# Optimization experiments

Measured on AMD Instinct MI355X. Metric: run time of the kernel, lower is better.

## Reference

```python
import jax, jax.numpy as jnp
from jax import lax
import numpy as np

B, H, W = 16, 512, 512
OPENING_R, EROSION_R, DILATION_R = 5, 2, 1
MIN_SIZE, AREA_THRESHOLD = 2000, 300
INF = np.int32(2 ** 30)


def _disk(r):
    # skimage.morphology.disk: x^2 + y^2 <= r^2 on a (2r+1)^2 grid
    y, x = np.mgrid[-r:r + 1, -r:r + 1]
    return jnp.asarray((x * x + y * y <= r * r).astype(np.float32))


D_OPEN, D_ERODE, D_DILATE = _disk(OPENING_R), _disk(EROSION_R), _disk(DILATION_R)


def _conv2(x, k):
    return lax.conv_general_dilated(x[None, None], k[None, None], (1, 1), 'VALID')[0, 0]


def _erode(fg, se):
    # skimage binary_erosion uses border_value=True (image border does not erode)
    r = se.shape[0] // 2
    x = jnp.pad(fg.astype(jnp.float32), r, constant_values=1.0)
    return _conv2(x, se) >= se.sum() - 0.5


def _dilate(fg, se):
    # skimage binary_dilation uses border_value=False
    r = se.shape[0] // 2
    x = jnp.pad(fg.astype(jnp.float32), r, constant_values=0.0)
    return _conv2(x, se) > 0.5


def _seg_cummin(v, reset, axis, reverse):
    # segmented cumulative-min: scan resets wherever `reset` is True (background)
    def comb(a, b):
        av, af = a
        bv, bf = b
        return jnp.where(bf, bv, jnp.minimum(av, bv)), af | bf

    vv, _ = lax.associative_scan(comb, (v, reset), axis=axis, reverse=reverse)
    return vv


def _label(fg):
    # 4-connectivity connected-component labeling via min-label propagation.
    # Each fg pixel starts with its raveled index; alternating row/col segmented
    # cummin sweeps run under while_loop until a fixed point (root id per comp).
    h, w = fg.shape
    idx = jnp.arange(h * w, dtype=jnp.int32).reshape(h, w)
    lab0 = jnp.where(fg, idx, INF)
    bg = ~fg

    def sweep(l):
        for axis in (1, 0):
            for rev in (False, True):
                l = jnp.where(fg, _seg_cummin(l, bg, axis, rev), INF)
        return l

    def body(c):
        l, _ = c
        nl = sweep(l)
        return nl, jnp.array_equal(nl, l)

    lab, _ = lax.while_loop(lambda c: ~c[1], body, (lab0, jnp.array(False)))
    seg = jnp.where(fg, lab, 0).ravel()
    sizes = jax.ops.segment_sum(fg.astype(jnp.int32).ravel(), seg, num_segments=h * w)
    ncomp = jnp.sum(sizes > 0)
    return lab, sizes, ncomp


def _remove_small_objects(fg, min_size, guard):
    lab, sizes, ncomp = _label(fg)
    px = sizes[jnp.where(fg, lab, 0)]  # component size at every fg pixel
    kept = fg & (px >= min_size)
    # original only removes small objects when label(...).max() > 1
    return jnp.where(ncomp > 1, kept, fg) if guard else kept


def _pipeline(mask):
    fg = mask > 0
    fg = _remove_small_objects(fg, MIN_SIZE, True)
    # remove_small_holes == ~remove_small_objects(~fg, area_threshold + 1)
    fg = ~_remove_small_objects(~fg, AREA_THRESHOLD + 1, False)
    fg = _erode(fg, D_ERODE)
    fg = _dilate(_erode(fg, D_OPEN), D_OPEN)  # binary_opening
    fg = _remove_small_objects(fg, MIN_SIZE, True)
    fg = _dilate(fg, D_DILATE)
    return fg.astype(jnp.float32)  # original casts to int; float32 kept for vjp parity


def setup_inputs() -> dict:
    key = jax.random.key(0)
    # blobby binary masks: threshold bilinearly-upsampled low-res noise so that
    # realistic large connected components (> min_size px) exist
    low = jax.random.uniform(key, (B, H // 16, W // 16), dtype=jnp.float32)
    blob = jax.image.resize(low, (B, H, W), method='bilinear')
    return {'inputs': (blob > 0.5).astype(jnp.float32)}


def reference(inputs):
    return jax.vmap(_pipeline)(inputs)
```

## Files before the change

### kernel.cpp

```cpp
#include <hip/hip_runtime.h>
#include <stdint.h>

#define BATCH 16
#define H 512
#define W 512
#define HW (H * W)
#define NTOT (BATCH * HW)
#define NWORDS (NTOT / 64)

#define SROWS 16
#define SWORDS 128
#define SPIX 8192
#define NSTRIPS (NWORDS / SWORDS)
#define IMG_STRIPS 32

#define MAXR 4096
#define NR (NSTRIPS * MAXR)

#define SPIN_LIMIT (1 << 20)

__device__ int g_flags[BATCH * 32];

__device__ __forceinline__ int ald(const int* p) {
    return __hip_atomic_load((int*)p, __ATOMIC_RELAXED, __HIP_MEMORY_SCOPE_AGENT);
}
__device__ __forceinline__ void ast(int* p, int v) {
    __hip_atomic_store(p, v, __ATOMIC_RELAXED, __HIP_MEMORY_SCOPE_AGENT);
}
__device__ __forceinline__ uint64_t ald64(const uint64_t* p) {
    return __hip_atomic_load((uint64_t*)p, __ATOMIC_RELAXED, __HIP_MEMORY_SCOPE_AGENT);
}
__device__ __forceinline__ void ast64(uint64_t* p, uint64_t v) {
    __hip_atomic_store(p, v, __ATOMIC_RELAXED, __HIP_MEMORY_SCOPE_AGENT);
}

__device__ __forceinline__ int find_root_c(int* L, int x) {
    int r = x, p = ald(&L[r]);
    while (p != r) { r = p; p = ald(&L[r]); }
    if (ald(&L[x]) != r) atomicMin(&L[x], r);
    return r;
}

__device__ void merge_uf(int* L, int a, int b) {
    while (true) {
        a = find_root_c(L, a);
        b = find_root_c(L, b);
        if (a == b) return;
        int lo = a < b ? a : b;
        int hi = a < b ? b : a;
        int old = atomicMin(&L[hi], lo);
        if (old == hi) return;
        a = lo; b = old;
    }
}

__device__ __forceinline__ int find_root_lds(int* P, int x) {
    int r = x, p = P[r];
    while (p != r) { r = p; p = P[r]; }
    return r;
}

__device__ void merge_lds(int* P, int a, int b) {
    while (true) {
        a = find_root_lds(P, a);
        b = find_root_lds(P, b);
        if (a == b) return;
        int lo = a < b ? a : b;
        int hi = a < b ? b : a;
        int old = atomicMin(&P[hi], lo);
        if (old == hi) return;
        a = lo; b = old;
    }
}

__device__ __forceinline__ int run_of(uint64_t m, int i, int cvrid, int wr) {
    uint64_t below = i ? ((~m) & ((1ull << i) - 1)) : 0ull;
    if (below == 0) return (cvrid >= 0) ? cvrid : wr;
    int s = 64 - __builtin_clzll(below);
    uint64_t starts = m & ~((m << 1) | ((cvrid >= 0) ? 1ull : 0ull));
    return wr + __popcll(starts & ((1ull << s) - 1));
}

__device__ __forceinline__ int run_of_lds(uint64_t m, int i, int cvrid,
                                          uint64_t starts, int wb) {
    uint64_t below = i ? ((~m) & ((1ull << i) - 1)) : 0ull;
    if (below == 0) return (cvrid >= 0) ? cvrid : wb;
    int s = 64 - __builtin_clzll(below);
    return wb + __popcll(starts & ((1ull << s) - 1));
}

__device__ __forceinline__ void hash_add(int* hk, int* hv, int* sizes,
                                         int r, int cnt) {
    uint32_t h = ((uint32_t)r * 2654435761u) >> 25;
    for (int tt = 0; tt < 16; ++tt) {
        int slot = (h + tt) & 127;
        int k = hk[slot];
        if (k == -1) k = atomicCAS(&hk[slot], -1, r);
        if (k == -1 || k == r) { atomicAdd(&hv[slot], cnt); return; }
    }
    atomicAdd(&sizes[r], cnt);
}

__device__ uint64_t keep_core(uint64_t m, int cvg, int wrg, int nc,
                              const int* L, const int* sizes, int minsz) {
    uint64_t res = m;
    if (!m) return res;
    uint64_t rem = m;
    uint64_t pc[4]; int rd[4];
    int rk = 0;
#pragma unroll
    for (int k = 0; k < 4; ++k) {
        pc[k] = 0; rd[k] = wrg;
        if (rem) {
            int s = __builtin_ctzll(rem);
            uint64_t rest = rem >> s;
            uint64_t nr = ~rest;
            int len = nr ? __builtin_ctzll(nr) : (64 - s);
            uint64_t piece = ((len >= 64) ? ~0ull : ((1ull << len) - 1)) << s;
            bool initial = !(s == 0 && cvg >= 0);
            pc[k] = piece;
            rd[k] = initial ? (wrg + rk) : cvg;
            rk += initial ? 1 : 0;
            rem &= ~piece;
        }
    }
    int rt[4], sz[4];
#pragma unroll
    for (int k = 0; k < 4; ++k) rt[k] = ald(&L[rd[k]]);
#pragma unroll
    for (int k = 0; k < 4; ++k) {
        int idx = pc[k] ? rt[k] : rd[k];
        sz[k] = ald(&sizes[idx]);
    }
    if (nc > 1) {
#pragma unroll
        for (int k = 0; k < 4; ++k)
            if (pc[k] && sz[k] < minsz) res &= ~pc[k];
        while (rem) {
            int s = __builtin_ctzll(rem);
            uint64_t rest = rem >> s;
            uint64_t nr = ~rest;
            int len = nr ? __builtin_ctzll(nr) : (64 - s);
            uint64_t piece = ((len >= 64) ? ~0ull : ((1ull << len) - 1)) << s;
            int rid = wrg + rk++;
            if (ald(&sizes[ald(&L[rid])]) < minsz) res &= ~piece;
            rem &= ~piece;
        }
    }
    return res;
}

__device__ uint64_t fill_core(uint64_t fg, int cvg, int wrg,
                              const int* L, const int* sizes, int minsz) {
    uint64_t bg = ~fg;
    uint64_t res = fg;
    if (!bg) return res;
    uint64_t rem = bg;
    uint64_t pc[4]; int rd[4];
    int rk = 0;
#pragma unroll
    for (int k = 0; k < 4; ++k) {
        pc[k] = 0; rd[k] = wrg;
        if (rem) {
            int s = __builtin_ctzll(rem);
            uint64_t rest = rem >> s;
            uint64_t nr = ~rest;
            int len = nr ? __builtin_ctzll(nr) : (64 - s);
            uint64_t piece = ((len >= 64) ? ~0ull : ((1ull << len) - 1)) << s;
            bool initial = !(s == 0 && cvg >= 0);
            pc[k] = piece;
            rd[k] = initial ? (wrg + rk) : cvg;
            rk += initial ? 1 : 0;
            rem &= ~piece;
        }
    }
    int rt[4], sz[4];
#pragma unroll
    for (int k = 0; k < 4; ++k) rt[k] = ald(&L[rd[k]]);
#pragma unroll
    for (int k = 0; k < 4; ++k) {
        int idx = pc[k] ? rt[k] : rd[k];
        sz[k] = ald(&sizes[idx]);
    }
#pragma unroll
    for (int k = 0; k < 4; ++k)
        if (pc[k] && sz[k] < minsz) res |= pc[k];
    while (rem) {
        int s = __builtin_ctzll(rem);
        uint64_t rest = rem >> s;
        uint64_t nr = ~rest;
        int len = nr ? __builtin_ctzll(nr) : (64 - s);
        uint64_t piece = ((len >= 64) ? ~0ull : ((1ull << len) - 1)) << s;
        int rid = wrg + rk++;
        if (ald(&sizes[ald(&L[rid])]) < minsz) res |= piece;
        rem &= ~piece;
    }
    return res;
}

__device__ void flatten_fast(uint64_t m, int cvg, int wrg,
                             int* L, int* sizes, int* ncomp_img,
                             int t, int* hk, int* hv) {
    if (t < 128) { hk[t] = -1; hv[t] = 0; }
    __syncthreads();
    if (t < SWORDS && m) {
        uint64_t rem = m;
        uint64_t pc[4]; int rd[4]; bool ini[4];
        int rk = 0;
#pragma unroll
        for (int k = 0; k < 4; ++k) {
            pc[k] = 0; rd[k] = wrg; ini[k] = false;
            if (rem) {
                int s = __builtin_ctzll(rem);
                uint64_t rest = rem >> s;
                uint64_t nr = ~rest;
                int len = nr ? __builtin_ctzll(nr) : (64 - s);
                uint64_t piece = ((len >= 64) ? ~0ull : ((1ull << len) - 1)) << s;
                bool initial = !(s == 0 && cvg >= 0);
                pc[k] = piece;
                rd[k] = initial ? (wrg + rk) : cvg;
                ini[k] = initial;
                rk += initial ? 1 : 0;
                rem &= ~piece;
            }
        }
        int h1[4], h2[4];
#pragma unroll
        for (int k = 0; k < 4; ++k) h1[k] = ald(&L[rd[k]]);
#pragma unroll
        for (int k = 0; k < 4; ++k) {
            int i1 = pc[k] ? h1[k] : rd[k];
            h2[k] = ald(&L[i1]);
        }
#pragma unroll
        for (int k = 0; k < 4; ++k) {
            if (pc[k]) {
                int r;
                if (h2[k] == h1[k]) r = h1[k];
                else {
                    r = h2[k];
                    int p = ald(&L[r]);
                    while (p != r) { r = p; p = ald(&L[r]); }
                }
                if (h1[k] != r) atomicMin(&L[rd[k]], r);
                if (ini[k] && r == rd[k]) atomicAdd(ncomp_img, 1);
                hash_add(hk, hv, sizes, r, __popcll(pc[k]));
            }
        }
        while (rem) {
            int s = __builtin_ctzll(rem);
            uint64_t rest = rem >> s;
            uint64_t nr = ~rest;
            int len = nr ? __builtin_ctzll(nr) : (64 - s);
            uint64_t piece = ((len >= 64) ? ~0ull : ((1ull << len) - 1)) << s;
            int rid = wrg + rk++;
            int r = find_root_c(L, rid);
            if (r == rid) atomicAdd(ncomp_img, 1);
            hash_add(hk, hv, sizes, r, __popcll(piece));
            rem &= ~piece;
        }
    }
    __syncthreads();
    if (t < 128 && hk[t] != -1) atomicAdd(&sizes[hk[t]], hv[t]);
}

template <int R, bool ERODE>
__device__ uint64_t morph_word_lds(const uint64_t* buf, int lrow, int w, int gyTop) {
    const uint64_t BORDER = ERODE ? ~0ull : 0ull;
    uint64_t res = ERODE ? ~0ull : 0ull;
#pragma unroll
    for (int dy = -R; dy <= R; ++dy) {
        int lr = lrow + dy;
        int gy = gyTop + lr;
        if (gy < 0 || gy >= H) continue;
        int v = R * R - dy * dy;
        int kx = 0;
        while ((kx + 1) * (kx + 1) <= v) ++kx;
        uint64_t cur = buf[lr * 8 + w];
        uint64_t prv = (w > 0) ? buf[lr * 8 + w - 1] : BORDER;
        uint64_t nxt = (w < 7) ? buf[lr * 8 + w + 1] : BORDER;
        uint64_t acc = cur;
#pragma unroll
        for (int dx = 1; dx <= kx; ++dx) {
            uint64_t right = (cur >> dx) | (nxt << (64 - dx));
            uint64_t left  = (cur << dx) | (prv >> (64 - dx));
            if (ERODE) acc &= right & left;
            else       acc |= right | left;
        }
        if (ERODE) res &= acc;
        else       res |= acc;
    }
    return res;
}

__device__ void strip_ccl_body(uint64_t m, uint64_t* sw, int* scarry,
                               int* cntL, int* wbL, int* par,
                               int blk, int t,
                               int* __restrict__ carry, int* __restrict__ wordrun,
                               int* __restrict__ L, int* __restrict__ sizes,
                               int* __restrict__ ncomp) {
    if (t < SWORDS) sw[t] = m;
    __syncthreads();

    if (t < SWORDS) {
        bool cont = (t & 7) ? ((sw[t - 1] >> 63) != 0) : false;
        int c = __popcll(m & ~(m << 1));
        if ((m & 1ull) && cont) --c;
        cntL[t] = c;
        wbL[t] = c;
    }
    __syncthreads();
    for (int off = 1; off < SWORDS; off <<= 1) {
        int v = 0;
        if (t < SWORDS && t >= off) v = wbL[t - off];
        __syncthreads();
        if (t < SWORDS) wbL[t] += v;
        __syncthreads();
    }

    if (t < SROWS) {
        int cv = -1;
        for (int i = 0; i < 8; ++i) {
            int lw = t * 8 + i;
            scarry[lw] = cv;
            uint64_t w = sw[lw];
            if (w >> 63) { if (cntL[lw] > 0) cv = wbL[lw] - 1; }
            else cv = -1;
        }
    }
    for (int i = t; i < MAXR; i += 256) par[i] = i;
    __syncthreads();

    int cv = -1, wb = 0;
    uint64_t starts = 0ull;
    if (t < SWORDS) {
        cv = scarry[t];
        wb = wbL[t] - cntL[t];
        ast(&carry[blk * SWORDS + t], (cv >= 0) ? (blk * MAXR + cv) : -1);
        ast(&wordrun[blk * SWORDS + t], blk * MAXR + wb);
        starts = m & ~((m << 1) | ((cv >= 0) ? 1ull : 0ull));
    }
    __syncthreads();

    if (t >= 8 && t < SWORDS && m) {
        uint64_t up = sw[t - 8];
        uint64_t cand = m & up;
        if (cand) {
            uint64_t curprev = (t & 7) ? sw[t - 1] : 0ull;
            uint64_t upprev  = (t & 7) ? sw[t - 9] : 0ull;
            uint64_t curl = (m << 1) | (curprev >> 63);
            uint64_t upl  = (up << 1) | (upprev >> 63);
            cand &= ~(curl & upl);
            int cvu = scarry[t - 8];
            int wbu = wbL[t - 8] - cntL[t - 8];
            uint64_t startsU = up & ~((up << 1) | ((cvu >= 0) ? 1ull : 0ull));
            while (cand) {
                int i = __builtin_ctzll(cand);
                int sP = run_of_lds(m, i, cv, starts, wb);
                int sQ = run_of_lds(up, i, cvu, startsU, wbu);
                merge_lds(par, sP, sQ);
                cand &= cand - 1;
            }
        }
    }
    __syncthreads();

    if (t < SWORDS) {
        int g = blk * MAXR;
        uint64_t ss = starts;
        int rk = 0;
        while (ss) {
            int rid = wb + rk; ++rk;
            int r = find_root_lds(par, rid);
            ast(&L[g + rid], g + r);
            if (r == rid) ast(&sizes[g + rid], 0);
            ss &= ss - 1;
        }
    }
    if (t == 0 && (blk & 31) == 0) ast(&ncomp[blk >> 5], 0);
}

__device__ __forceinline__ void ibar(int img, int si, int ep, int phase) {
    int* base = g_flags + img * 32;
    __syncthreads();
    if (threadIdx.x == 0) {
        asm volatile("s_waitcnt vmcnt(0)" ::: "memory");
        ast(&base[si], ep + phase);
    }
    if (threadIdx.x < 32) {
        int spins = 0;
        while (ald(&base[threadIdx.x]) - ep < phase && ++spins < SPIN_LIMIT)
            __builtin_amdgcn_s_sleep(1);
    }
    __syncthreads();
}

__global__ __launch_bounds__(256, 2) void k_mega(
        const float4* __restrict__ in4, float* __restrict__ out,
        int* LA, int* sizesA, int* LB, int* sizesB,
        uint64_t* bits1, uint64_t* bits2, uint64_t* bits3,
        int* carryA, int* carryB, int* wordrunA, int* wordrunB,
        int* ncompA, int* ncompB) {
    __shared__ uint64_t sw[SWORDS];
    __shared__ int scarry[SWORDS];
    __shared__ int cntL[SWORDS];
    __shared__ int wbL[SWORDS];
    __shared__ union US {
        int par[MAXR];
        struct { uint64_t A[320]; uint64_t B[320]; } mo;
        struct { int hk[128]; int hv[128]; } ha;
        struct { uint64_t kb[80]; uint64_t db[64]; } kd;
    } U;
    int blk = blockIdx.x;
    int t = threadIdx.x;
    int img = blk >> 5, si = blk & 31;
    int ep = ald(&g_flags[img * 32 + si]);

#pragma unroll
    for (int it = 0; it < 8; ++it) {
        int q = blk * (SPIX / 4) + it * 256 + t;
        float4 v = in4[q];
        uint32_t nib = (v.x > 0.0f ? 1u : 0u) | (v.y > 0.0f ? 2u : 0u) |
                       (v.z > 0.0f ? 4u : 0u) | (v.w > 0.0f ? 8u : 0u);
        uint64_t val = (uint64_t)nib << (4 * (t & 15));
        val |= __shfl_xor(val, 1);
        val |= __shfl_xor(val, 2);
        val |= __shfl_xor(val, 4);
        val |= __shfl_xor(val, 8);
        if ((t & 15) == 0) {
            ast64(&bits1[q >> 4], val);
            sw[it * 16 + (t >> 4)] = val;
        }
    }
    __syncthreads();

    {
        uint64_t m = (t < SWORDS) ? sw[t] : 0ull;
        strip_ccl_body(m, sw, scarry, cntL, wbL, U.par, blk, t,
                       carryA, wordrunA, LA, sizesA, ncompA);
    }
    ibar(img, si, ep, 1);

    if (t < 8 && si < 31) {
        int gw = (blk + 1) * SWORDS + t;
        uint64_t cur = ald64(&bits1[gw]);
        uint64_t curprev = t ? ald64(&bits1[gw - 1]) : 0ull;
        int cvc = ald(&carryA[gw]);
        int wrc = ald(&wordrunA[gw]);
        uint64_t up = sw[120 + t];
        uint64_t upprev = t ? sw[119 + t] : 0ull;
        int cvuL = scarry[120 + t];
        int cvu = cvuL >= 0 ? blk * MAXR + cvuL : -1;
        int wru = blk * MAXR + (wbL[120 + t] - cntL[120 + t]);
        uint64_t cand = cur & up;
        if (cand) {
            uint64_t curl = (cur << 1) | (curprev >> 63);
            uint64_t upl  = (up << 1) | (upprev >> 63);
            cand &= ~(curl & upl);
            while (cand) {
                int i = __builtin_ctzll(cand);
                int sP = run_of(cur, i, cvc, wrc);
                int sQ = run_of(up, i, cvu, wru);
                merge_uf(LA, sP, sQ);
                cand &= cand - 1;
            }
        }
    }
    ibar(img, si, ep, 2);

    {
        uint64_t m = (t < SWORDS) ? sw[t] : 0ull;
        int cvL = (t < SWORDS) ? scarry[t] : -1;
        int cvg = cvL >= 0 ? blk * MAXR + cvL : -1;
        int wrg = blk * MAXR + ((t < SWORDS) ? (wbL[t] - cntL[t]) : 0);
        flatten_fast(m, cvg, wrg, LA, sizesA, &ncompA[img], t, U.ha.hk, U.ha.hv);
    }
    ibar(img, si, ep, 3);

    {
        uint64_t m2 = 0ull;
        if (t < SWORDS) {
            int nc = ald(&ncompA[img]);
            uint64_t m1 = sw[t];
            int cvL = scarry[t];
            int cvg = cvL >= 0 ? blk * MAXR + cvL : -1;
            int wrg = blk * MAXR + (wbL[t] - cntL[t]);
            uint64_t kw = keep_core(m1, cvg, wrg, nc, LA, sizesA, 2000);
            ast64(&bits2[blk * SWORDS + t], kw);
            m2 = ~kw;
        }
        strip_ccl_body(m2, sw, scarry, cntL, wbL, U.par, blk, t,
                       carryB, wordrunB, LB, sizesB, ncompB);
    }
    ibar(img, si, ep, 4);

    if (t < 8 && si < 31) {
        int gw = (blk + 1) * SWORDS + t;
        uint64_t cur = ~ald64(&bits2[gw]);
        uint64_t curprev = t ? ~ald64(&bits2[gw - 1]) : 0ull;
        int cvc = ald(&carryB[gw]);
        int wrc = ald(&wordrunB[gw]);
        uint64_t up = sw[120 + t];
        uint64_t upprev = t ? sw[119 + t] : 0ull;
        int cvuL = scarry[120 + t];
        int cvu = cvuL >= 0 ? blk * MAXR + cvuL : -1;
        int wru = blk * MAXR + (wbL[120 + t] - cntL[120 + t]);
        uint64_t cand = cur & up;
        if (cand) {
            uint64_t curl = (cur << 1) | (curprev >> 63);
            uint64_t upl  = (up << 1) | (upprev >> 63);
            cand &= ~(curl & upl);
            while (cand) {
                int i = __builtin_ctzll(cand);
                int sP = run_of(cur, i, cvc, wrc);
                int sQ = run_of(up, i, cvu, wru);
                merge_uf(LB, sP, sQ);
                cand &= cand - 1;
            }
        }
    }
    ibar(img, si, ep, 5);

    {
        uint64_t m = (t < SWORDS) ? sw[t] : 0ull;
        int cvL = (t < SWORDS) ? scarry[t] : -1;
        int cvg = cvL >= 0 ? blk * MAXR + cvL : -1;
        int wrg = blk * MAXR + ((t < SWORDS) ? (wbL[t] - cntL[t]) : 0);
        flatten_fast(m, cvg, wrg, LB, sizesB, &ncompB[img], t, U.ha.hk, U.ha.hv);
    }
    ibar(img, si, ep, 6);

    {
        int gyTop = si * 16 - 12;
        for (int lw = t; lw < 320; lw += 256) {
            int gy = gyTop + (lw >> 3);
            int w = lw & 7;
            uint64_t v = 0;
            if (gy >= 0 && gy < H) {
                uint64_t fg; int cvg, wrg;
                if (lw >= 96 && lw < 224) {
                    int ti = lw - 96;
                    fg = ~sw[ti];
                    int cvL = scarry[ti];
                    cvg = cvL >= 0 ? blk * MAXR + cvL : -1;
                    wrg = blk * MAXR + (wbL[ti] - cntL[ti]);
                } else {
                    int gw = img * 4096 + gy * 8 + w;
                    fg = ald64(&bits2[gw]);
                    cvg = ald(&carryB[gw]);
                    wrg = ald(&wordrunB[gw]);
                }
                v = fill_core(fg, cvg, wrg, LB, sizesB, 301);
            }
            U.mo.A[lw] = v;
        }
        __syncthreads();
        for (int lw = t; lw < 320; lw += 256) {
            int lr = lw >> 3;
            if (lr >= 2 && lr <= 37) U.mo.B[lw] = morph_word_lds<2, true>(U.mo.A, lr, lw & 7, gyTop);
        }
        __syncthreads();
        for (int lw = t; lw < 320; lw += 256) {
            int lr = lw >> 3;
            if (lr >= 7 && lr <= 32) U.mo.A[lw] = morph_word_lds<5, true>(U.mo.B, lr, lw & 7, gyTop);
        }
        __syncthreads();
        for (int lw = t; lw < 320; lw += 256) {
            int lr = lw >> 3;
            if (lr >= 12 && lr <= 27) U.mo.B[lw] = morph_word_lds<5, false>(U.mo.A, lr, lw & 7, gyTop);
        }
        __syncthreads();
        uint64_t m3 = 0ull;
        if (t < SWORDS) {
            m3 = U.mo.B[t + 96];
            ast64(&bits3[blk * SWORDS + t], m3);
        }
        strip_ccl_body(m3, sw, scarry, cntL, wbL, U.par, blk, t,
                       carryA, wordrunA, LA, sizesA, ncompA);
    }
    ibar(img, si, ep, 7);

    if (t < 8 && si < 31) {
        int gw = (blk + 1) * SWORDS + t;
        uint64_t cur = ald64(&bits3[gw]);
        uint64_t curprev = t ? ald64(&bits3[gw - 1]) : 0ull;
        int cvc = ald(&carryA[gw]);
        int wrc = ald(&wordrunA[gw]);
        uint64_t up = sw[120 + t];
        uint64_t upprev = t ? sw[119 + t] : 0ull;
        int cvuL = scarry[120 + t];
        int cvu = cvuL >= 0 ? blk * MAXR + cvuL : -1;
        int wru = blk * MAXR + (wbL[120 + t] - cntL[120 + t]);
        uint64_t cand = cur & up;
        if (cand) {
            uint64_t curl = (cur << 1) | (curprev >> 63);
            uint64_t upl  = (up << 1) | (upprev >> 63);
            cand &= ~(curl & upl);
            while (cand) {
                int i = __builtin_ctzll(cand);
                int sP = run_of(cur, i, cvc, wrc);
                int sQ = run_of(up, i, cvu, wru);
                merge_uf(LA, sP, sQ);
                cand &= cand - 1;
            }
        }
    }
    ibar(img, si, ep, 8);

    {
        uint64_t m = (t < SWORDS) ? sw[t] : 0ull;
        int cvL = (t < SWORDS) ? scarry[t] : -1;
        int cvg = cvL >= 0 ? blk * MAXR + cvL : -1;
        int wrg = blk * MAXR + ((t < SWORDS) ? (wbL[t] - cntL[t]) : 0);
        flatten_fast(m, cvg, wrg, LA, sizesA, &ncompA[img], t, U.ha.hk, U.ha.hv);
    }
    ibar(img, si, ep, 9);

    for (int k = 0; k < 2; ++k) {
        int s8 = 2 * si + k;
        int y0 = s8 * 8;
        if (t < 80) {
            int lr = t >> 3, w = t & 7;
            int gy = y0 - 1 + lr;
            uint64_t v = 0;
            if (gy >= 0 && gy < H) {
                int nc = ald(&ncompA[img]);
                uint64_t m; int cvg, wrg;
                int rel = gy - 16 * si;
                if (rel >= 0 && rel < 16) {
                    int ti = rel * 8 + w;
                    m = sw[ti];
                    int cvL = scarry[ti];
                    cvg = cvL >= 0 ? blk * MAXR + cvL : -1;
                    wrg = blk * MAXR + (wbL[ti] - cntL[ti]);
                } else {
                    int gw = img * 4096 + gy * 8 + w;
                    m = ald64(&bits3[gw]);
                    cvg = ald(&carryA[gw]);
                    wrg = ald(&wordrunA[gw]);
                }
                v = keep_core(m, cvg, wrg, nc, LA, sizesA, 2000);
            }
            U.kd.kb[t] = v;
        }
        __syncthreads();
        if (t < 64) {
            int r = t >> 3, w = t & 7;
            uint64_t cur = U.kd.kb[(r + 1) * 8 + w];
            uint64_t up  = U.kd.kb[r * 8 + w];
            uint64_t dn  = U.kd.kb[(r + 2) * 8 + w];
            uint64_t prv = w ? U.kd.kb[(r + 1) * 8 + w - 1] : 0ull;
            uint64_t nxt = (w < 7) ? U.kd.kb[(r + 1) * 8 + w + 1] : 0ull;
            U.kd.db[t] = cur | up | dn | (cur << 1) | (prv >> 63) |
                         (cur >> 1) | (nxt << 63);
        }
        __syncthreads();
        {
            int q0 = t * 16;
            uint64_t wd = U.kd.db[q0 >> 6];
            int sh = q0 & 63;
            float4* o = (float4*)(out + (size_t)img * HW + (size_t)y0 * W + q0);
#pragma unroll
            for (int kk = 0; kk < 4; ++kk) {
                uint32_t nib = (uint32_t)(wd >> (sh + kk * 4)) & 0xFu;
                float4 f;
                f.x = (nib & 1u) ? 1.0f : 0.0f;
                f.y = (nib & 2u) ? 1.0f : 0.0f;
                f.z = (nib & 4u) ? 1.0f : 0.0f;
                f.w = (nib & 8u) ? 1.0f : 0.0f;
                o[kk] = f;
            }
        }
        __syncthreads();
    }
}

extern "C" void kernel_launch(void* const* d_in, const int* in_sizes, int n_in,
                              void* d_out, int out_size, void* d_ws, size_t ws_size,
                              hipStream_t stream) {
    const float* in = (const float*)d_in[0];
    float* out = (float*)d_out;

    uint8_t* ws = (uint8_t*)d_ws;
    int* LA      = (int*)ws;
    int* sizesA  = LA + NR;
    int* LB      = sizesA + NR;
    int* sizesB  = LB + NR;
    uint64_t* bits1 = (uint64_t*)(sizesB + NR);
    uint64_t* bits2 = bits1 + NWORDS;
    uint64_t* bits3 = bits2 + NWORDS;
    int* carryA   = (int*)(bits3 + NWORDS);
    int* carryB   = carryA + NWORDS;
    int* wordrunA = carryB + NWORDS;
    int* wordrunB = wordrunA + NWORDS;
    int* ncompA   = wordrunB + NWORDS;
    int* ncompB   = ncompA + BATCH;

    k_mega<<<NSTRIPS, 256, 0, stream>>>((const float4*)in, out,
                                        LA, sizesA, LB, sizesB,
                                        bits1, bits2, bits3,
                                        carryA, carryB, wordrunA, wordrunB,
                                        ncompA, ncompB);
}
```

Before: 189.8 us.

## Keep local union-find parents in LDS and cache per-root sizes in shared hash

The strip-local parent array now has its own shared-memory buffer and survives past the local CCL step. Flattening, keep and fill passes resolve each run's local root in LDS and look up its global root and size through a 256-slot shared hash. The hash is filled once per strip, replacing per-run global loads of labels and sizes. Halo rows keep the global path. Bounded walk limits were added to the find loops. The cost is extra LDS footprint that may lower occupancy, plus more barriers.

```diff
diff --git a/kernel.cpp b/kernel.cpp
--- a/kernel.cpp
+++ b/kernel.cpp
@@ -18,6 +18,7 @@
 #define NR (NSTRIPS * MAXR)
 
 #define SPIN_LIMIT (1 << 20)
+#define WALK_LIMIT (1 << 16)
 
 __device__ int g_flags[BATCH * 32];
 
@@ -35,14 +36,21 @@
 }
 
 __device__ __forceinline__ int find_root_c(int* L, int x) {
-    int r = x, p = ald(&L[r]);
-    while (p != r) { r = p; p = ald(&L[r]); }
+    int r = x, p = ald(&L[r]), g = 0;
+    while (p != r && ++g < WALK_LIMIT) { r = p; p = ald(&L[r]); }
     if (ald(&L[x]) != r) atomicMin(&L[x], r);
     return r;
 }
 
+__device__ __forceinline__ int walk_root(const int* L, int x) {
+    int r = x, p = ald(&L[r]), g = 0;
+    while (p != r && ++g < WALK_LIMIT) { r = p; p = ald(&L[r]); }
+    return r;
+}
+
 __device__ void merge_uf(int* L, int a, int b) {
-    while (true) {
+    int g = 0;
+    while (++g < WALK_LIMIT) {
         a = find_root_c(L, a);
         b = find_root_c(L, b);
         if (a == b) return;
@@ -54,14 +62,15 @@
     }
 }
 
-__device__ __forceinline__ int find_root_lds(int* P, int x) {
-    int r = x, p = P[r];
-    while (p != r) { r = p; p = P[r]; }
+__device__ __forceinline__ int find_root_lds(const int* P, int x) {
+    int r = x, p = P[r], g = 0;
+    while (p != r && ++g < WALK_LIMIT) { r = p; p = P[r]; }
     return r;
 }
 
 __device__ void merge_lds(int* P, int a, int b) {
-    while (true) {
+    int g = 0;
+    while (++g < WALK_LIMIT) {
         a = find_root_lds(P, a);
         b = find_root_lds(P, b);
         if (a == b) return;
@@ -89,179 +98,163 @@
     return wb + __popcll(starts & ((1ull << s) - 1));
 }
 
-__device__ __forceinline__ void hash_add(int* hk, int* hv, int* sizes,
-                                         int r, int cnt) {
-    uint32_t h = ((uint32_t)r * 2654435761u) >> 25;
-    for (int tt = 0; tt < 16; ++tt) {
-        int slot = (h + tt) & 127;
-        int k = hk[slot];
-        if (k == -1) k = atomicCAS(&hk[slot], -1, r);
-        if (k == -1 || k == r) { atomicAdd(&hv[slot], cnt); return; }
-    }
-    atomicAdd(&sizes[r], cnt);
-}
-
-__device__ uint64_t keep_core(uint64_t m, int cvg, int wrg, int nc,
-                              const int* L, const int* sizes, int minsz) {
-    uint64_t res = m;
-    if (!m) return res;
-    uint64_t rem = m;
-    uint64_t pc[4]; int rd[4];
-    int rk = 0;
-#pragma unroll
-    for (int k = 0; k < 4; ++k) {
-        pc[k] = 0; rd[k] = wrg;
-        if (rem) {
-            int s = __builtin_ctzll(rem);
-            uint64_t rest = rem >> s;
-            uint64_t nr = ~rest;
-            int len = nr ? __builtin_ctzll(nr) : (64 - s);
-            uint64_t piece = ((len >= 64) ? ~0ull : ((1ull << len) - 1)) << s;
-            bool initial = !(s == 0 && cvg >= 0);
-            pc[k] = piece;
-            rd[k] = initial ? (wrg + rk) : cvg;
-            rk += initial ? 1 : 0;
-            rem &= ~piece;
-        }
-    }
-    int rt[4], sz[4];
-#pragma unroll
-    for (int k = 0; k < 4; ++k) rt[k] = ald(&L[rd[k]]);
-#pragma unroll
-    for (int k = 0; k < 4; ++k) {
-        int idx = pc[k] ? rt[k] : rd[k];
-        sz[k] = ald(&sizes[idx]);
-    }
-    if (nc > 1) {
-#pragma unroll
-        for (int k = 0; k < 4; ++k)
-            if (pc[k] && sz[k] < minsz) res &= ~pc[k];
+__device__ __forceinline__ int hash_insert(int key, int cnt, int* hk, int* hcnt) {
+    uint32_t h = ((uint32_t)key * 2654435761u) >> 24;
+    for (int p = 0; p < 16; ++p) {
+        int s = (h + p) & 255;
+        int k = hk[s];
+        if (k == -1) k = atomicCAS(&hk[s], -1, key);
+        if (k == -1 || k == key) { atomicAdd(&hcnt[s], cnt); return s; }
+    }
+    return -1;
+}
+__device__ __forceinline__ int hash_find(int key, const int* hk) {
+    uint32_t h = ((uint32_t)key * 2654435761u) >> 24;
+    for (int p = 0; p < 16; ++p) {
+        int s = (h + p) & 255;
+        if (hk[s] == key) return s;
+        if (hk[s] == -1) return -1;
+    }
+    return -1;
+}
+
+__device__ void flatten_map(uint64_t m, int cvL, int wb, const int* par,
+                            int gbase, int* L, int* sizes, int* ncomp_img,
+                            int t, int* hk, int* hcnt, int* hrs) {
+    for (int i = t; i < 256; i += 256) { hk[i] = -1; hcnt[i] = 0; }
+    __syncthreads();
+    if (t < SWORDS && m) {
+        uint64_t rem = m; int rk = 0;
         while (rem) {
             int s = __builtin_ctzll(rem);
             uint64_t rest = rem >> s;
             uint64_t nr = ~rest;
             int len = nr ? __builtin_ctzll(nr) : (64 - s);
             uint64_t piece = ((len >= 64) ? ~0ull : ((1ull << len) - 1)) << s;
-            int rid = wrg + rk++;
-            if (ald(&sizes[ald(&L[rid])]) < minsz) res &= ~piece;
+            bool ini = !(s == 0 && cvL >= 0);
+            int rl = ini ? (wb + rk) : cvL; rk += ini ? 1 : 0;
+            int rloc = find_root_lds(par, rl);
+            int cnt = __popcll(piece);
+            if (hash_insert(rloc, cnt, hk, hcnt) < 0)
+                atomicAdd(&sizes[find_root_c(L, gbase + rloc)], cnt);
             rem &= ~piece;
         }
     }
-    return res;
-}
-
-__device__ uint64_t fill_core(uint64_t fg, int cvg, int wrg,
-                              const int* L, const int* sizes, int minsz) {
-    uint64_t bg = ~fg;
-    uint64_t res = fg;
-    if (!bg) return res;
-    uint64_t rem = bg;
-    uint64_t pc[4]; int rd[4];
-    int rk = 0;
-#pragma unroll
-    for (int k = 0; k < 4; ++k) {
-        pc[k] = 0; rd[k] = wrg;
-        if (rem) {
+    __syncthreads();
+    if (t < 256 && hk[t] != -1) {
+        int g = gbase + hk[t];
+        int r = find_root_c(L, g);
+        hrs[t] = r;
+        atomicAdd(&sizes[r], hcnt[t]);
+    }
+    __syncthreads();
+    if (t < SWORDS && m) {
+        uint64_t rem = m; int rk = 0;
+        while (rem) {
             int s = __builtin_ctzll(rem);
             uint64_t rest = rem >> s;
             uint64_t nr = ~rest;
             int len = nr ? __builtin_ctzll(nr) : (64 - s);
             uint64_t piece = ((len >= 64) ? ~0ull : ((1ull << len) - 1)) << s;
-            bool initial = !(s == 0 && cvg >= 0);
-            pc[k] = piece;
-            rd[k] = initial ? (wrg + rk) : cvg;
-            rk += initial ? 1 : 0;
+            bool ini = !(s == 0 && cvL >= 0);
+            if (ini) {
+                int rl = wb + rk;
+                int rloc = find_root_lds(par, rl);
+                int sl = hash_find(rloc, hk);
+                int r = (sl >= 0) ? hrs[sl] : walk_root(L, gbase + rloc);
+                ast(&L[gbase + rl], r);
+                if (r == gbase + rl) atomicAdd(ncomp_img, 1);
+                ++rk;
+            }
             rem &= ~piece;
         }
     }
-    int rt[4], sz[4];
-#pragma unroll
-    for (int k = 0; k < 4; ++k) rt[k] = ald(&L[rd[k]]);
-#pragma unroll
-    for (int k = 0; k < 4; ++k) {
-        int idx = pc[k] ? rt[k] : rd[k];
-        sz[k] = ald(&sizes[idx]);
-    }
-#pragma unroll
-    for (int k = 0; k < 4; ++k)
-        if (pc[k] && sz[k] < minsz) res |= pc[k];
+}
+
+__device__ __forceinline__ void preload_sv(const int* sizes, int t,
+                                           const int* hk, const int* hrs, int* hsv) {
+    if (t < 256 && hk[t] != -1) hsv[t] = ald(&sizes[hrs[t]]);
+}
+
+__device__ uint64_t keep_map(uint64_t m, int cvL, int wb, const int* par, int gbase,
+                             const int* L, const int* sizes, int minsz,
+                             const int* hk, const int* hrs, const int* hsv) {
+    uint64_t res = m, rem = m; int rk = 0;
     while (rem) {
         int s = __builtin_ctzll(rem);
         uint64_t rest = rem >> s;
         uint64_t nr = ~rest;
         int len = nr ? __builtin_ctzll(nr) : (64 - s);
         uint64_t piece = ((len >= 64) ? ~0ull : ((1ull << len) - 1)) << s;
-        int rid = wrg + rk++;
-        if (ald(&sizes[ald(&L[rid])]) < minsz) res |= piece;
+        bool ini = !(s == 0 && cvL >= 0);
+        int rl = ini ? (wb + rk) : cvL; rk += ini ? 1 : 0;
+        int rloc = find_root_lds(par, rl);
+        int sl = hash_find(rloc, hk);
+        int sz = (sl >= 0) ? hsv[sl] : ald(&sizes[walk_root(L, gbase + rloc)]);
+        if (sz < minsz) res &= ~piece;
         rem &= ~piece;
     }
     return res;
 }
 
-__device__ void flatten_fast(uint64_t m, int cvg, int wrg,
-                             int* L, int* sizes, int* ncomp_img,
-                             int t, int* hk, int* hv) {
-    if (t < 128) { hk[t] = -1; hv[t] = 0; }
-    __syncthreads();
-    if (t < SWORDS && m) {
-        uint64_t rem = m;
-        uint64_t pc[4]; int rd[4]; bool ini[4];
-        int rk = 0;
-#pragma unroll
-        for (int k = 0; k < 4; ++k) {
-            pc[k] = 0; rd[k] = wrg; ini[k] = false;
-            if (rem) {
-                int s = __builtin_ctzll(rem);
-                uint64_t rest = rem >> s;
-                uint64_t nr = ~rest;
-                int len = nr ? __builtin_ctzll(nr) : (64 - s);
-                uint64_t piece = ((len >= 64) ? ~0ull : ((1ull << len) - 1)) << s;
-                bool initial = !(s == 0 && cvg >= 0);
-                pc[k] = piece;
-                rd[k] = initial ? (wrg + rk) : cvg;
-                ini[k] = initial;
-                rk += initial ? 1 : 0;
-                rem &= ~piece;
-            }
-        }
-        int h1[4], h2[4];
-#pragma unroll
-        for (int k = 0; k < 4; ++k) h1[k] = ald(&L[rd[k]]);
-#pragma unroll
-        for (int k = 0; k < 4; ++k) {
-            int i1 = pc[k] ? h1[k] : rd[k];
-            h2[k] = ald(&L[i1]);
-        }
-#pragma unroll
-        for (int k = 0; k < 4; ++k) {
-            if (pc[k]) {
-                int r;
-                if (h2[k] == h1[k]) r = h1[k];
-                else {
-                    r = h2[k];
-                    int p = ald(&L[r]);
-                    while (p != r) { r = p; p = ald(&L[r]); }
-                }
-                if (h1[k] != r) atomicMin(&L[rd[k]], r);
-                if (ini[k] && r == rd[k]) atomicAdd(ncomp_img, 1);
-                hash_add(hk, hv, sizes, r, __popcll(pc[k]));
-            }
-        }
+__device__ uint64_t fill_map(uint64_t fg, int cvL, int wb, const int* par, int gbase,
+                             const int* L, const int* sizes, int minsz,
+                             const int* hk, const int* hrs, const int* hsv) {
+    uint64_t bg = ~fg;
+    uint64_t res = fg, rem = bg; int rk = 0;
+    while (rem) {
+        int s = __builtin_ctzll(rem);
+        uint64_t rest = rem >> s;
+        uint64_t nr = ~rest;
+        int len = nr ? __builtin_ctzll(nr) : (64 - s);
+        uint64_t piece = ((len >= 64) ? ~0ull : ((1ull << len) - 1)) << s;
+        bool ini = !(s == 0 && cvL >= 0);
+        int rl = ini ? (wb + rk) : cvL; rk += ini ? 1 : 0;
+        int rloc = find_root_lds(par, rl);
+        int sl = hash_find(rloc, hk);
+        int sz = (sl >= 0) ? hsv[sl] : ald(&sizes[walk_root(L, gbase + rloc)]);
+        if (sz < minsz) res |= piece;
+        rem &= ~piece;
+    }
+    return res;
+}
+
+__device__ uint64_t keep_halo(uint64_t m, int cvg, int wrg, int nc,
+                              const int* L, const int* sizes, int minsz) {
+    uint64_t res = m;
+    if (m && nc > 1) {
+        uint64_t rem = m; int rk = 0;
         while (rem) {
             int s = __builtin_ctzll(rem);
             uint64_t rest = rem >> s;
             uint64_t nr = ~rest;
             int len = nr ? __builtin_ctzll(nr) : (64 - s);
             uint64_t piece = ((len >= 64) ? ~0ull : ((1ull << len) - 1)) << s;
-            int rid = wrg + rk++;
-            int r = find_root_c(L, rid);
-            if (r == rid) atomicAdd(ncomp_img, 1);
-            hash_add(hk, hv, sizes, r, __popcll(piece));
+            bool ini = !(s == 0 && cvg >= 0);
+            int rid = ini ? (wrg + rk) : cvg; rk += ini ? 1 : 0;
+            if (ald(&sizes[ald(&L[rid])]) < minsz) res &= ~piece;
             rem &= ~piece;
         }
     }
-    __syncthreads();
-    if (t < 128 && hk[t] != -1) atomicAdd(&sizes[hk[t]], hv[t]);
+    return res;
+}
+__device__ uint64_t fill_halo(uint64_t fg, int cvg, int wrg,
+                              const int* L, const int* sizes, int minsz) {
+    uint64_t bg = ~fg;
+    uint64_t res = fg;
+    uint64_t rem = bg; int rk = 0;
+    while (rem) {
+        int s = __builtin_ctzll(rem);
+        uint64_t rest = rem >> s;
+        uint64_t nr = ~rest;
+        int len = nr ? __builtin_ctzll(nr) : (64 - s);
+        uint64_t piece = ((len >= 64) ? ~0ull : ((1ull << len) - 1)) << s;
+        bool ini = !(s == 0 && cvg >= 0);
+        int rid = ini ? (wrg + rk) : cvg; rk += ini ? 1 : 0;
+        if (ald(&sizes[ald(&L[rid])]) < minsz) res |= piece;
+        rem &= ~piece;
+    }
+    return res;
 }
 
 template <int R, bool ERODE>
@@ -405,15 +398,17 @@
     __shared__ int scarry[SWORDS];
     __shared__ int cntL[SWORDS];
     __shared__ int wbL[SWORDS];
+    __shared__ int hk[256], hcnt[256], hrs[256], hsv[256];
+    __shared__ int shnc;
+    __shared__ int parS[MAXR];
     __shared__ union US {
-        int par[MAXR];
         struct { uint64_t A[320]; uint64_t B[320]; } mo;
-        struct { int hk[128]; int hv[128]; } ha;
         struct { uint64_t kb[80]; uint64_t db[64]; } kd;
     } U;
     int blk = blockIdx.x;
     int t = threadIdx.x;
     int img = blk >> 5, si = blk & 31;
+    int gb = blk * MAXR;
     int ep = ald(&g_flags[img * 32 + si]);
 
 #pragma unroll
@@ -436,7 +431,7 @@
 
     {
         uint64_t m = (t < SWORDS) ? sw[t] : 0ull;
-        strip_ccl_body(m, sw, scarry, cntL, wbL, U.par, blk, t,
+        strip_ccl_body(m, sw, scarry, cntL, wbL, parS, blk, t,
                        carryA, wordrunA, LA, sizesA, ncompA);
     }
     ibar(img, si, ep, 1);
@@ -450,8 +445,8 @@
         uint64_t up = sw[120 + t];
         uint64_t upprev = t ? sw[119 + t] : 0ull;
         int cvuL = scarry[120 + t];
-        int cvu = cvuL >= 0 ? blk * MAXR + cvuL : -1;
-        int wru = blk * MAXR + (wbL[120 + t] - cntL[120 + t]);
+        int cvu = cvuL >= 0 ? gb + cvuL : -1;
+        int wru = gb + (wbL[120 + t] - cntL[120 + t]);
         uint64_t cand = cur & up;
         if (cand) {
             uint64_t curl = (cur << 1) | (curprev >> 63);
@@ -471,25 +466,29 @@
     {
         uint64_t m = (t < SWORDS) ? sw[t] : 0ull;
         int cvL = (t < SWORDS) ? scarry[t] : -1;
-        int cvg = cvL >= 0 ? blk * MAXR + cvL : -1;
-        int wrg = blk * MAXR + ((t < SWORDS) ? (wbL[t] - cntL[t]) : 0);
-        flatten_fast(m, cvg, wrg, LA, sizesA, &ncompA[img], t, U.ha.hk, U.ha.hv);
+        int wb = (t < SWORDS) ? (wbL[t] - cntL[t]) : 0;
+        flatten_map(m, cvL, wb, parS, gb, LA, sizesA, &ncompA[img],
+                    t, hk, hcnt, hrs);
     }
     ibar(img, si, ep, 3);
 
     {
+        if (t == 0) shnc = ald(&ncompA[img]);
+        preload_sv(sizesA, t, hk, hrs, hsv);
+        __syncthreads();
         uint64_t m2 = 0ull;
         if (t < SWORDS) {
-            int nc = ald(&ncompA[img]);
             uint64_t m1 = sw[t];
             int cvL = scarry[t];
-            int cvg = cvL >= 0 ? blk * MAXR + cvL : -1;
-            int wrg = blk * MAXR + (wbL[t] - cntL[t]);
-            uint64_t kw = keep_core(m1, cvg, wrg, nc, LA, sizesA, 2000);
+            int wb = wbL[t] - cntL[t];
+            uint64_t kw = (shnc > 1)
+                ? keep_map(m1, cvL, wb, parS, gb, LA, sizesA, 2000, hk, hrs, hsv)
+                : m1;
             ast64(&bits2[blk * SWORDS + t], kw);
             m2 = ~kw;
         }
-        strip_ccl_body(m2, sw, scarry, cntL, wbL, U.par, blk, t,
+        __syncthreads();
+        strip_ccl_body(m2, sw, scarry, cntL, wbL, parS, blk, t,
                        carryB, wordrunB, LB, sizesB, ncompB);
     }
     ibar(img, si, ep, 4);
@@ -503,8 +502,8 @@
         uint64_t up = sw[120 + t];
         uint64_t upprev = t ? sw[119 + t] : 0ull;
         int cvuL = scarry[120 + t];
-        int cvu = cvuL >= 0 ? blk * MAXR + cvuL : -1;
-        int wru = blk * MAXR + (wbL[120 + t] - cntL[120 + t]);
+        int cvu = cvuL >= 0 ? gb + cvuL : -1;
+        int wru = gb + (wbL[120 + t] - cntL[120 + t]);
         uint64_t cand = cur & up;
         if (cand) {
             uint64_t curl = (cur << 1) | (curprev >> 63);
@@ -524,33 +523,35 @@
     {
         uint64_t m = (t < SWORDS) ? sw[t] : 0ull;
         int cvL = (t < SWORDS) ? scarry[t] : -1;
-        int cvg = cvL >= 0 ? blk * MAXR + cvL : -1;
-        int wrg = blk * MAXR + ((t < SWORDS) ? (wbL[t] - cntL[t]) : 0);
-        flatten_fast(m, cvg, wrg, LB, sizesB, &ncompB[img], t, U.ha.hk, U.ha.hv);
+        int wb = (t < SWORDS) ? (wbL[t] - cntL[t]) : 0;
+        flatten_map(m, cvL, wb, parS, gb, LB, sizesB, &ncompB[img],
+                    t, hk, hcnt, hrs);
     }
     ibar(img, si, ep, 6);
 
     {
+        preload_sv(sizesB, t, hk, hrs, hsv);
+        __syncthreads();
         int gyTop = si * 16 - 12;
         for (int lw = t; lw < 320; lw += 256) {
             int gy = gyTop + (lw >> 3);
             int w = lw & 7;
             uint64_t v = 0;
             if (gy >= 0 && gy < H) {
-                uint64_t fg; int cvg, wrg;
                 if (lw >= 96 && lw < 224) {
                     int ti = lw - 96;
-                    fg = ~sw[ti];
+                    uint64_t fg = ~sw[ti];
                     int cvL = scarry[ti];
-                    cvg = cvL >= 0 ? blk * MAXR + cvL : -1;
-                    wrg = blk * MAXR + (wbL[ti] - cntL[ti]);
+                    int wb = wbL[ti] - cntL[ti];
+                    v = fill_map(fg, cvL, wb, parS, gb, LB, sizesB, 301,
+                                 hk, hrs, hsv);
                 } else {
                     int gw = img * 4096 + gy * 8 + w;
-                    fg = ald64(&bits2[gw]);
-                    cvg = ald(&carryB[gw]);
-                    wrg = ald(&wordrunB[gw]);
+                    uint64_t fg = ald64(&bits2[gw]);
+                    int cvg = ald(&carryB[gw]);
+                    int wrg = ald(&wordrunB[gw]);
+                    v = fill_halo(fg, cvg, wrg, LB, sizesB, 301);
                 }
-                v = fill_core(fg, cvg, wrg, LB, sizesB, 301);
             }
             U.mo.A[lw] = v;
         }
@@ -575,7 +576,8 @@
             m3 = U.mo.B[t + 96];
             ast64(&bits3[blk * SWORDS + t], m3);
         }
-        strip_ccl_body(m3, sw, scarry, cntL, wbL, U.par, blk, t,
+        __syncthreads();
+        strip_ccl_body(m3, sw, scarry, cntL, wbL, parS, blk, t,
                        carryA, wordrunA, LA, sizesA, ncompA);
     }
     ibar(img, si, ep, 7);
@@ -589,8 +591,8 @@
         uint64_t up = sw[120 + t];
         uint64_t upprev = t ? sw[119 + t] : 0ull;
         int cvuL = scarry[120 + t];
-        int cvu = cvuL >= 0 ? blk * MAXR + cvuL : -1;
-        int wru = blk * MAXR + (wbL[120 + t] - cntL[120 + t]);
+        int cvu = cvuL >= 0 ? gb + cvuL : -1;
+        int wru = gb + (wbL[120 + t] - cntL[120 + t]);
         uint64_t cand = cur & up;
         if (cand) {
             uint64_t curl = (cur << 1) | (curprev >> 63);
@@ -610,68 +612,74 @@
     {
         uint64_t m = (t < SWORDS) ? sw[t] : 0ull;
         int cvL = (t < SWORDS) ? scarry[t] : -1;
-        int cvg = cvL >= 0 ? blk * MAXR + cvL : -1;
-        int wrg = blk * MAXR + ((t < SWORDS) ? (wbL[t] - cntL[t]) : 0);
-        flatten_fast(m, cvg, wrg, LA, sizesA, &ncompA[img], t, U.ha.hk, U.ha.hv);
+        int wb = (t < SWORDS) ? (wbL[t] - cntL[t]) : 0;
+        flatten_map(m, cvL, wb, parS, gb, LA, sizesA, &ncompA[img],
+                    t, hk, hcnt, hrs);
     }
     ibar(img, si, ep, 9);
 
-    for (int k = 0; k < 2; ++k) {
-        int s8 = 2 * si + k;
-        int y0 = s8 * 8;
-        if (t < 80) {
-            int lr = t >> 3, w = t & 7;
-            int gy = y0 - 1 + lr;
-            uint64_t v = 0;
-            if (gy >= 0 && gy < H) {
-                int nc = ald(&ncompA[img]);
-                uint64_t m; int cvg, wrg;
-                int rel = gy - 16 * si;
-                if (rel >= 0 && rel < 16) {
-                    int ti = rel * 8 + w;
-                    m = sw[ti];
-                    int cvL = scarry[ti];
-                    cvg = cvL >= 0 ? blk * MAXR + cvL : -1;
-                    wrg = blk * MAXR + (wbL[ti] - cntL[ti]);
-                } else {
-                    int gw = img * 4096 + gy * 8 + w;
-                    m = ald64(&bits3[gw]);
-                    cvg = ald(&carryA[gw]);
-                    wrg = ald(&wordrunA[gw]);
+    {
+        if (t == 0) shnc = ald(&ncompA[img]);
+        preload_sv(sizesA, t, hk, hrs, hsv);
+        __syncthreads();
+        for (int k = 0; k < 2; ++k) {
+            int s8 = 2 * si + k;
+            int y0 = s8 * 8;
+            if (t < 80) {
+                int lr = t >> 3, w = t & 7;
+                int gy = y0 - 1 + lr;
+                uint64_t v = 0;
+                if (gy >= 0 && gy < H) {
+                    int rel = gy - 16 * si;
+                    if (rel >= 0 && rel < 16) {
+                        int ti = rel * 8 + w;
+                        uint64_t m = sw[ti];
+                        int cvL = scarry[ti];
+                        int wb = wbL[ti] - cntL[ti];
+                        v = (shnc > 1)
+                            ? keep_map(m, cvL, wb, parS, gb, LA, sizesA, 2000,
+                                       hk, hrs, hsv)
+                            : m;
+                    } else {
+                        int gw = img * 4096 + gy * 8 + w;
+                        uint64_t m = ald64(&bits3[gw]);
+                        int cvg = ald(&carryA[gw]);
+                        int wrg = ald(&wordrunA[gw]);
+                        v = keep_halo(m, cvg, wrg, shnc, LA, sizesA, 2000);
+                    }
                 }
-                v = keep_core(m, cvg, wrg, nc, LA, sizesA, 2000);
-            }
-            U.kd.kb[t] = v;
-        }
-        __syncthreads();
-        if (t < 64) {
-            int r = t >> 3, w = t & 7;
-            uint64_t cur = U.kd.kb[(r + 1) * 8 + w];
-            uint64_t up  = U.kd.kb[r * 8 + w];
-            uint64_t dn  = U.kd.kb[(r + 2) * 8 + w];
-            uint64_t prv = w ? U.kd.kb[(r + 1) * 8 + w - 1] : 0ull;
-            uint64_t nxt = (w < 7) ? U.kd.kb[(r + 1) * 8 + w + 1] : 0ull;
-            U.kd.db[t] = cur | up | dn | (cur << 1) | (prv >> 63) |
-                         (cur >> 1) | (nxt << 63);
-        }
-        __syncthreads();
-        {
-            int q0 = t * 16;
-            uint64_t wd = U.kd.db[q0 >> 6];
-            int sh = q0 & 63;
-            float4* o = (float4*)(out + (size_t)img * HW + (size_t)y0 * W + q0);
+                U.kd.kb[t] = v;
+            }
+            __syncthreads();
+            if (t < 64) {
+                int r = t >> 3, w = t & 7;
+                uint64_t cur = U.kd.kb[(r + 1) * 8 + w];
+                uint64_t up  = U.kd.kb[r * 8 + w];
+                uint64_t dn  = U.kd.kb[(r + 2) * 8 + w];
+                uint64_t prv = w ? U.kd.kb[(r + 1) * 8 + w - 1] : 0ull;
+                uint64_t nxt = (w < 7) ? U.kd.kb[(r + 1) * 8 + w + 1] : 0ull;
+                U.kd.db[t] = cur | up | dn | (cur << 1) | (prv >> 63) |
+                             (cur >> 1) | (nxt << 63);
+            }
+            __syncthreads();
+            {
+                int q0 = t * 16;
+                uint64_t wd = U.kd.db[q0 >> 6];
+                int sh = q0 & 63;
+                float4* o = (float4*)(out + (size_t)img * HW + (size_t)y0 * W + q0);
 #pragma unroll
-            for (int kk = 0; kk < 4; ++kk) {
-                uint32_t nib = (uint32_t)(wd >> (sh + kk * 4)) & 0xFu;
-                float4 f;
-                f.x = (nib & 1u) ? 1.0f : 0.0f;
-                f.y = (nib & 2u) ? 1.0f : 0.0f;
-                f.z = (nib & 4u) ? 1.0f : 0.0f;
-                f.w = (nib & 8u) ? 1.0f : 0.0f;
-                o[kk] = f;
-            }
-        }
-        __syncthreads();
+                for (int kk = 0; kk < 4; ++kk) {
+                    uint32_t nib = (uint32_t)(wd >> (sh + kk * 4)) & 0xFu;
+                    float4 f;
+                    f.x = (nib & 1u) ? 1.0f : 0.0f;
+                    f.y = (nib & 2u) ? 1.0f : 0.0f;
+                    f.z = (nib & 4u) ? 1.0f : 0.0f;
+                    f.w = (nib & 8u) ? 1.0f : 0.0f;
+                    o[kk] = f;
+                }
+            }
+            __syncthreads();
+        }
     }
 }
 
```

New measurement: 193.9 us. 2.2% more time.
